# Kernel tuning notes

Hardware: AMD Instinct MI355X
Metric: run time of the kernel (lower is better)

## Reference

```python
import jax, jax.numpy as jnp
import numpy as np

EMB = 1024   # embedding_size = input_size // 2
HID = 1024   # hidden_size
B = 16384


def _glorot(key, shape):
    fan_in = shape[0]
    bound = 1.0 / np.sqrt(fan_in)
    return jax.random.uniform(key, shape, jnp.float32, -bound, bound)


def setup_inputs() -> dict:
    key = jax.random.key(0)
    ks = jax.random.split(key, 14)
    return {
        "inputs": jax.random.normal(ks[0], (B, 2 * EMB), jnp.float32),
        "state": jax.random.normal(ks[1], (B, HID), jnp.float32),
        # weights stored [in, out] (transpose of torch Linear layout)
        "Wr": _glorot(ks[2], (EMB + HID, HID)), "br": jnp.zeros((HID,), jnp.float32),
        "Wu": _glorot(ks[3], (EMB + HID, HID)), "bu": jnp.zeros((HID,), jnp.float32),
        "Wc": _glorot(ks[4], (EMB + HID, HID)), "bc": jnp.zeros((HID,), jnp.float32),
        "W1": _glorot(ks[5], (EMB, HID)), "b1": jnp.zeros((HID,), jnp.float32),
        "W2": _glorot(ks[6], (EMB, HID)), "b2": jnp.zeros((HID,), jnp.float32),
        "Wg": _glorot(ks[7], (2 * HID, HID)), "bg": jnp.zeros((HID,), jnp.float32),
    }


def reference(inputs, state, Wr, br, Wu, bu, Wc, bc, W1, b1, W2, b2, Wg, bg):
    # split input into semantic half and neighbor half
    x = inputs[:, :EMB]          # [B, EMB]
    neighbors = inputs[:, EMB:]  # [B, EMB]

    gate_inputs = jnp.concatenate([x, state], axis=1)            # [B, EMB+HID]
    r = jax.nn.sigmoid(gate_inputs @ Wr + br)                    # reset gate
    u = jax.nn.sigmoid(gate_inputs @ Wu + bu)                    # update gate
    c = jnp.tanh(jnp.concatenate([x, r * state], axis=1) @ Wc + bc)

    semantic_emb = jax.nn.relu(x @ W1 + b1)
    neighbor_emb = jax.nn.relu(neighbors @ W2 + b2)
    new_gate = jax.nn.sigmoid(
        jnp.concatenate([semantic_emb, neighbor_emb], axis=1) @ Wg + bg)

    new_h = u * state + (1.0 - u) * c * new_gate
    return new_h
```

## Files before the change

### kernel.cpp

```cpp
#include <hip/hip_runtime.h>
#include <hip/hip_bf16.h>
#include <math.h>

#define Bsz 16384
#define HIDc 1024

typedef __attribute__((ext_vector_type(8))) short short8_t;
typedef __attribute__((ext_vector_type(4))) float f32x4;
typedef __attribute__((ext_vector_type(4))) short s16x4;

typedef __attribute__((address_space(1))) const unsigned char* gp1_t;
typedef __attribute__((address_space(3))) unsigned char* lp3_t;

__device__ __forceinline__ float sigf(float x) { return 1.0f / (1.0f + __expf(-x)); }
__device__ __forceinline__ float tanh_fast(float x) {
  x = fminf(fmaxf(x, -10.f), 10.f);
  float t = __expf(2.f * x);
  return (t - 1.f) / (t + 1.f);
}

__device__ __forceinline__ int xcd_map(int bid, int nwg) {
  const int q = nwg >> 3, r = nwg & 7;
  const int xcd = bid & 7, idx = bid >> 3;
  return (xcd < r ? xcd * (q + 1) : r * (q + 1) + (xcd - r) * q) + idx;
}

#define DSR(dst, addr, IMM) \
  asm volatile("ds_read_b128 %0, %1 offset:" IMM : "=v"(dst) : "v"(addr))

#define STAGE_ADV(BUFB) do {                                                                     \
    __hip_bfloat16* db_ = lds + (BUFB);                                                          \
    __builtin_amdgcn_global_load_lds((gp1_t)pa0, (lp3_t)(db_ + tid * 8), 16, 0, 0);              \
    __builtin_amdgcn_global_load_lds((gp1_t)pa1, (lp3_t)(db_ + (512 + tid) * 8), 16, 0, 0);      \
    __builtin_amdgcn_global_load_lds((gp1_t)pa2, (lp3_t)(db_ + (1024 + tid) * 8), 16, 0, 0);     \
    __builtin_amdgcn_global_load_lds((gp1_t)pa3, (lp3_t)(db_ + (1536 + tid) * 8), 16, 0, 0);     \
    __builtin_amdgcn_global_load_lds((gp1_t)pb0, (lp3_t)(db_ + 16384 + tid * 8), 16, 0, 0);      \
    __builtin_amdgcn_global_load_lds((gp1_t)pb1, (lp3_t)(db_ + 16384 + (512 + tid) * 8), 16, 0, 0); \
    __builtin_amdgcn_global_load_lds((gp1_t)pb2, (lp3_t)(db_ + 16384 + (1024 + tid) * 8), 16, 0, 0); \
    __builtin_amdgcn_global_load_lds((gp1_t)pb3, (lp3_t)(db_ + 16384 + (1536 + tid) * 8), 16, 0, 0); \
    pa0 += 64; pa1 += 64; pa2 += 64; pa3 += 64;                                                  \
    pb0 += 64; pb1 += 64; pb2 += 64; pb3 += 64;                                                  \
  } while (0)

template <int EPI>
__global__ __launch_bounds__(512, 2)
void gemm256(const __hip_bfloat16* __restrict__ A, long lda,
             const __hip_bfloat16* __restrict__ Wt, long ldw, int nbx,
             const float* __restrict__ bias0, const float* __restrict__ bias1,
             const __hip_bfloat16* __restrict__ stbf,
             const __hip_bfloat16* __restrict__ auxbf,
             const __hip_bfloat16* __restrict__ CB,
             const __hip_bfloat16* __restrict__ U,
             __hip_bfloat16* __restrict__ out0,
             __hip_bfloat16* __restrict__ out1,
             float* __restrict__ outf) {
  constexpr int KC = (EPI == 0 || EPI == 4) ? 2048 : 1024;
  constexpr int NS = KC / 64;
  __shared__ __hip_bfloat16 lds[2 * 32768];

  const int tid = threadIdx.x;
  const int wave = tid >> 6, lane = tid & 63;
  const int wr = wave >> 2, wc = wave & 3;
  const int lm = lane & 15, hi = lane >> 4, l7 = lane & 7;

  const int wg = xcd_map(blockIdx.x, gridDim.x);
  const long mBase = (long)(wg / nbx) * 256;
  const long nBase = (long)(wg % nbx) * 256;
  const __hip_bfloat16* Ablk = A + mBase * lda;
  const __hip_bfloat16* Wblk = Wt + nBase * ldw;

  const __hip_bfloat16 *pa0, *pa1, *pa2, *pa3, *pb0, *pb1, *pb2, *pb3;
  {
    const int s0 = tid, s1 = 512 + tid, s2 = 1024 + tid, s3 = 1536 + tid;
    const int r0 = s0 >> 3, r1 = s1 >> 3, r2 = s2 >> 3, r3 = s3 >> 3;
    const int c0 = ((s0 & 7) ^ (r0 & 7)) << 3, c1 = ((s1 & 7) ^ (r1 & 7)) << 3;
    const int c2 = ((s2 & 7) ^ (r2 & 7)) << 3, c3 = ((s3 & 7) ^ (r3 & 7)) << 3;
    pa0 = Ablk + (long)r0 * lda + c0;  pa1 = Ablk + (long)r1 * lda + c1;
    pa2 = Ablk + (long)r2 * lda + c2;  pa3 = Ablk + (long)r3 * lda + c3;
    pb0 = Wblk + (long)r0 * ldw + c0;  pb1 = Wblk + (long)r1 * ldw + c1;
    pb2 = Wblk + (long)r2 * ldw + c2;  pb3 = Wblk + (long)r3 * ldw + c3;
  }

  const unsigned ldsbase = (unsigned)(size_t)(void*)lds;
  const unsigned laneA = (unsigned)((wr * 128 + lm) * 128 + ((hi ^ l7) << 4));
  const unsigned laneB = (unsigned)(32768 + (wc * 64 + lm) * 128 + ((hi ^ l7) << 4));

  f32x4 acc[8][4];
#pragma unroll
  for (int m = 0; m < 8; ++m)
#pragma unroll
    for (int n = 0; n < 4; ++n) acc[m][n] = (f32x4){0.f, 0.f, 0.f, 0.f};

  STAGE_ADV(0);
  STAGE_ADV(32768);

#pragma unroll 1
  for (int s = 0; s < NS; ++s) {
    if (s == NS - 1) asm volatile("s_waitcnt vmcnt(0)" ::: "memory");
    else             asm volatile("s_waitcnt vmcnt(8)" ::: "memory");
    __builtin_amdgcn_s_barrier();

    const unsigned base = ldsbase + (unsigned)((s & 1) * 65536);
    const unsigned a0 = base + laneA, b0 = base + laneB;
    const unsigned a1 = a0 ^ 64u, b1 = b0 ^ 64u;
    short8_t a8[8], b8[4];

    DSR(a8[0], a0, "0");    DSR(a8[1], a0, "2048");  DSR(a8[2], a0, "4096");
    DSR(a8[3], a0, "6144"); DSR(a8[4], a0, "8192");  DSR(a8[5], a0, "10240");
    DSR(a8[6], a0, "12288");DSR(a8[7], a0, "14336");
    DSR(b8[0], b0, "0");    DSR(b8[1], b0, "2048");  DSR(b8[2], b0, "4096");
    DSR(b8[3], b0, "6144");
    asm volatile("s_waitcnt lgkmcnt(0)" ::: "memory");
    __builtin_amdgcn_sched_barrier(0);
    __builtin_amdgcn_s_setprio(1);
#pragma unroll
    for (int mf = 0; mf < 8; ++mf)
#pragma unroll
      for (int nf = 0; nf < 4; ++nf)
        acc[mf][nf] = __builtin_amdgcn_mfma_f32_16x16x32_bf16(a8[mf], b8[nf],
                                                              acc[mf][nf], 0, 0, 0);
    __builtin_amdgcn_s_setprio(0);

    DSR(a8[0], a1, "0");    DSR(a8[1], a1, "2048");  DSR(a8[2], a1, "4096");
    DSR(a8[3], a1, "6144"); DSR(a8[4], a1, "8192");  DSR(a8[5], a1, "10240");
    DSR(a8[6], a1, "12288");DSR(a8[7], a1, "14336");
    DSR(b8[0], b1, "0");    DSR(b8[1], b1, "2048");  DSR(b8[2], b1, "4096");
    DSR(b8[3], b1, "6144");
    asm volatile("s_waitcnt lgkmcnt(0)" ::: "memory");
    __builtin_amdgcn_sched_barrier(0);
    __builtin_amdgcn_s_barrier();
    __builtin_amdgcn_sched_barrier(0);
    if (s + 2 < NS) STAGE_ADV((s & 1) * 32768);
    __builtin_amdgcn_s_setprio(1);
#pragma unroll
    for (int mf = 0; mf < 8; ++mf)
#pragma unroll
      for (int nf = 0; nf < 4; ++nf)
        acc[mf][nf] = __builtin_amdgcn_mfma_f32_16x16x32_bf16(a8[mf], b8[nf],
                                                              acc[mf][nf], 0, 0, 0);
    __builtin_amdgcn_s_setprio(0);
  }

#pragma unroll
  for (int mf = 0; mf < 8; ++mf)
#pragma unroll
    for (int nf = 0; nf < 4; ++nf)
#pragma unroll
      for (int j = 0; j < 4; ++j) {
        const long row = mBase + wr * 128 + mf * 16 + hi * 4 + j;
        const int col = (int)nBase + wc * 64 + nf * 16 + lm;
        const float v = acc[mf][nf][j];
        if (EPI == 0) {
          if (col < HIDc) {
            float rr = sigf(v + bias0[col]);
            float st = __bfloat162float(stbf[row * 2048 + 1024 + col]);
            out0[row * HIDc + col] = __float2bfloat16(rr * st);
          } else {
            int c = col - HIDc;
            out1[row * HIDc + c] = __float2bfloat16(sigf(v + bias1[c]));
          }
        } else if (EPI == 1) {
          if (col < HIDc) {
            out0[row * 2048 + col] = __float2bfloat16(fmaxf(v + bias0[col], 0.f));
          } else {
            int c = col - HIDc;
            out1[row * HIDc + c] = __float2bfloat16(v + bias1[c]);
          }
        } else if (EPI == 2) {
          out0[row * 2048 + HIDc + col] = __float2bfloat16(fmaxf(v + bias0[col], 0.f));
        } else if (EPI == 3) {
          const long idx = row * HIDc + col;
          out0[idx] = __float2bfloat16(tanh_fast(v + __bfloat162float(auxbf[idx])));
        } else {
          const long idx = row * HIDc + col;
          float g = sigf(v + bias0[col]);
          float u = __bfloat162float(U[idx]);
          float cb = __bfloat162float(CB[idx]);
          float st = __bfloat162float(stbf[row * 2048 + 1024 + col]);
          outf[idx] = u * st + (1.f - u) * cb * g;
        }
      }
}

__global__ __launch_bounds__(256)
void prep_k(const float4* __restrict__ in4, const float4* __restrict__ st4,
            __hip_bfloat16* __restrict__ A1, __hip_bfloat16* __restrict__ NB,
            const float* __restrict__ Wr, const float* __restrict__ Wu,
            const float* __restrict__ W1, const float* __restrict__ Wc,
            const float* __restrict__ W2, const float* __restrict__ Wg,
            __hip_bfloat16* __restrict__ Wru_t, __hip_bfloat16* __restrict__ W1cx_t,
            __hip_bfloat16* __restrict__ Wcb_t, __hip_bfloat16* __restrict__ W2_t,
            __hip_bfloat16* __restrict__ Wg_t) {
  const int bid = blockIdx.x;
  if (bid < 10240) {
    const float* s_; __hip_bfloat16* d_; long ldo; int j, ktiles;
    if (bid < 2048)      { j = bid;        s_ = Wr; d_ = Wru_t;               ldo = 2048; ktiles = 64; }
    else if (bid < 4096) { j = bid - 2048; s_ = Wu; d_ = Wru_t + 1024L * 2048; ldo = 2048; ktiles = 64; }
    else if (bid < 5120) { j = bid - 4096; s_ = W1; d_ = W1cx_t;              ldo = 1024; ktiles = 32; }
    else if (bid < 6144) { j = bid - 5120; s_ = Wc; d_ = W1cx_t + 1024L * 1024; ldo = 1024; ktiles = 32; }
    else if (bid < 7168) { j = bid - 6144; s_ = Wc + 1024L * 1024; d_ = Wcb_t; ldo = 1024; ktiles = 32; }
    else if (bid < 8192) { j = bid - 7168; s_ = W2; d_ = W2_t;                ldo = 1024; ktiles = 32; }
    else                 { j = bid - 8192; s_ = Wg; d_ = Wg_t;                ldo = 2048; ktiles = 64; }
    const int k0 = (j % ktiles) * 32, n0 = (j / ktiles) * 32;
    __shared__ float t[32][33];
    const int tx = threadIdx.x & 31, ty = threadIdx.x >> 5;
#pragma unroll
    for (int dy = 0; dy < 32; dy += 8)
      t[ty + dy][tx] = s_[(long)(k0 + ty + dy) * 1024 + n0 + tx];
    __syncthreads();
#pragma unroll
    for (int dy = 0; dy < 32; dy += 8)
      d_[(long)(n0 + ty + dy) * ldo + k0 + tx] = __float2bfloat16(t[tx][ty + dy]);
  } else {
    const long NI4 = (long)Bsz * 2048 / 4;
    const long NS4 = (long)Bsz * 1024 / 4;
    for (long i = (long)(bid - 10240) * 256 + threadIdx.x; i < NI4 + NS4;
         i += 2048L * 256) {
      float4 v;
      __hip_bfloat16* dst;
      if (i < NI4) {
        v = in4[i];
        long e = i << 2;
        long row = e >> 11;
        int col = (int)(e & 2047);
        dst = (col < 1024) ? (A1 + row * 2048 + col) : (NB + row * 1024 + (col - 1024));
      } else {
        long jj = i - NI4;
        v = st4[jj];
        long e = jj << 2;
        long row = e >> 10;
        int col = (int)(e & 1023);
        dst = A1 + row * 2048 + 1024 + col;
      }
      union { __hip_bfloat16 h[4]; s16x4 s; } u;
      u.h[0] = __float2bfloat16(v.x);
      u.h[1] = __float2bfloat16(v.y);
      u.h[2] = __float2bfloat16(v.z);
      u.h[3] = __float2bfloat16(v.w);
      *reinterpret_cast<s16x4*>(dst) = u.s;
    }
  }
}

extern "C" void kernel_launch(void* const* d_in, const int* in_sizes, int n_in,
                              void* d_out, int out_size, void* d_ws, size_t ws_size,
                              hipStream_t stream) {
  const float* inputs = (const float*)d_in[0];
  const float* state = (const float*)d_in[1];
  const float* Wr = (const float*)d_in[2];
  const float* br = (const float*)d_in[3];
  const float* Wu = (const float*)d_in[4];
  const float* bu = (const float*)d_in[5];
  const float* Wc = (const float*)d_in[6];
  const float* bc = (const float*)d_in[7];
  const float* W1 = (const float*)d_in[8];
  const float* b1 = (const float*)d_in[9];
  const float* W2 = (const float*)d_in[10];
  const float* b2 = (const float*)d_in[11];
  const float* Wg = (const float*)d_in[12];
  const float* bg = (const float*)d_in[13];
  float* out = (float*)d_out;

  char* ws = (char*)d_ws;
  __hip_bfloat16* A1    = (__hip_bfloat16*)(ws);
  __hip_bfloat16* NB    = (__hip_bfloat16*)(ws + 67108864L);
  __hip_bfloat16* RS    = (__hip_bfloat16*)(ws + 100663296L);
  __hip_bfloat16* Ub    = (__hip_bfloat16*)(ws + 134217728L);
  __hip_bfloat16* SN    = (__hip_bfloat16*)(ws + 167772160L);
  __hip_bfloat16* CXb   = (__hip_bfloat16*)(ws + 234881024L);
  __hip_bfloat16* Wru_t = (__hip_bfloat16*)(ws + 268435456L);
  __hip_bfloat16* W1cx_t= (__hip_bfloat16*)(ws + 276824064L);
  __hip_bfloat16* Wcb_t = (__hip_bfloat16*)(ws + 281018368L);
  __hip_bfloat16* W2_t  = (__hip_bfloat16*)(ws + 283115520L);
  __hip_bfloat16* Wg_t  = (__hip_bfloat16*)(ws + 285212672L);
  __hip_bfloat16* CB    = NB;

  prep_k<<<12288, 256, 0, stream>>>((const float4*)inputs, (const float4*)state,
                                    A1, NB, Wr, Wu, W1, Wc, W2, Wg,
                                    Wru_t, W1cx_t, Wcb_t, W2_t, Wg_t);

  gemm256<0><<<512, 512, 0, stream>>>(A1, 2048, Wru_t, 2048, 8,
                                      br, bu, A1, nullptr, nullptr, nullptr,
                                      RS, Ub, nullptr);
  gemm256<1><<<512, 512, 0, stream>>>(A1, 2048, W1cx_t, 1024, 8,
                                      b1, bc, nullptr, nullptr, nullptr, nullptr,
                                      SN, CXb, nullptr);
  gemm256<2><<<256, 512, 0, stream>>>(NB, 1024, W2_t, 1024, 4,
                                      b2, nullptr, nullptr, nullptr, nullptr, nullptr,
                                      SN, nullptr, nullptr);
  gemm256<3><<<256, 512, 0, stream>>>(RS, 1024, Wcb_t, 1024, 4,
                                      nullptr, nullptr, nullptr, CXb, nullptr, nullptr,
                                      CB, nullptr, nullptr);
  gemm256<4><<<256, 512, 0, stream>>>(SN, 2048, Wg_t, 2048, 4,
                                      bg, nullptr, A1, nullptr, CB, Ub,
                                      nullptr, nullptr, out);
}
```

Before: 522.4 us.

## Split GEMM main loop into four quadrant MFMA phases with interleaved LDS reads

Restructures the K-loop of the 256x256 GEMM so each stage runs as four quadrant MFMA blocks (over M and N halves), each covering both K sub-steps. LDS fragment reads for the next quadrant sit between barriers, and the global prefetch is issued before the last quadrant. The aim is to overlap LDS reads with MFMA work across waves and to move the vmcnt wait to the end of the iteration. The cost is many more workgroup barriers per iteration and more live fragment registers.

```diff
diff --git a/kernel.cpp b/kernel.cpp
--- a/kernel.cpp
+++ b/kernel.cpp
@@ -40,6 +40,21 @@
     __builtin_amdgcn_global_load_lds((gp1_t)pb3, (lp3_t)(db_ + 16384 + (1536 + tid) * 8), 16, 0, 0); \
     pa0 += 64; pa1 += 64; pa2 += 64; pa3 += 64;                                                  \
     pb0 += 64; pb1 += 64; pb2 += 64; pb3 += 64;                                                  \
+  } while (0)
+
+#define MFMA_Q(QM, QN) do {                                                      \
+    asm volatile("s_waitcnt lgkmcnt(0)" ::: "memory");                           \
+    __builtin_amdgcn_sched_barrier(0);                                           \
+    __builtin_amdgcn_s_setprio(1);                                               \
+    _Pragma("unroll") for (int ks = 0; ks < 2; ++ks)                             \
+      _Pragma("unroll") for (int mf = 0; mf < 4; ++mf)                           \
+        _Pragma("unroll") for (int nf = 0; nf < 2; ++nf)                         \
+          acc[(QM) * 4 + mf][(QN) * 2 + nf] =                                    \
+              __builtin_amdgcn_mfma_f32_16x16x32_bf16(                           \
+                  a8[mf][ks], b8[QN][nf][ks],                                    \
+                  acc[(QM) * 4 + mf][(QN) * 2 + nf], 0, 0, 0);                   \
+    __builtin_amdgcn_s_setprio(0);                                               \
+    __builtin_amdgcn_sched_barrier(0);                                           \
   } while (0)
 
 template <int EPI>
@@ -91,54 +106,49 @@
 #pragma unroll
     for (int n = 0; n < 4; ++n) acc[m][n] = (f32x4){0.f, 0.f, 0.f, 0.f};
 
+  short8_t a8[4][2], b8[2][2][2];
+
   STAGE_ADV(0);
   STAGE_ADV(32768);
+  asm volatile("s_waitcnt vmcnt(8)" ::: "memory");
+  __builtin_amdgcn_s_barrier();
 
 #pragma unroll 1
   for (int s = 0; s < NS; ++s) {
-    if (s == NS - 1) asm volatile("s_waitcnt vmcnt(0)" ::: "memory");
-    else             asm volatile("s_waitcnt vmcnt(8)" ::: "memory");
-    __builtin_amdgcn_s_barrier();
-
     const unsigned base = ldsbase + (unsigned)((s & 1) * 65536);
     const unsigned a0 = base + laneA, b0 = base + laneB;
     const unsigned a1 = a0 ^ 64u, b1 = b0 ^ 64u;
-    short8_t a8[8], b8[4];
-
-    DSR(a8[0], a0, "0");    DSR(a8[1], a0, "2048");  DSR(a8[2], a0, "4096");
-    DSR(a8[3], a0, "6144"); DSR(a8[4], a0, "8192");  DSR(a8[5], a0, "10240");
-    DSR(a8[6], a0, "12288");DSR(a8[7], a0, "14336");
-    DSR(b8[0], b0, "0");    DSR(b8[1], b0, "2048");  DSR(b8[2], b0, "4096");
-    DSR(b8[3], b0, "6144");
-    asm volatile("s_waitcnt lgkmcnt(0)" ::: "memory");
-    __builtin_amdgcn_sched_barrier(0);
-    __builtin_amdgcn_s_setprio(1);
-#pragma unroll
-    for (int mf = 0; mf < 8; ++mf)
-#pragma unroll
-      for (int nf = 0; nf < 4; ++nf)
-        acc[mf][nf] = __builtin_amdgcn_mfma_f32_16x16x32_bf16(a8[mf], b8[nf],
-                                                              acc[mf][nf], 0, 0, 0);
-    __builtin_amdgcn_s_setprio(0);
-
-    DSR(a8[0], a1, "0");    DSR(a8[1], a1, "2048");  DSR(a8[2], a1, "4096");
-    DSR(a8[3], a1, "6144"); DSR(a8[4], a1, "8192");  DSR(a8[5], a1, "10240");
-    DSR(a8[6], a1, "12288");DSR(a8[7], a1, "14336");
-    DSR(b8[0], b1, "0");    DSR(b8[1], b1, "2048");  DSR(b8[2], b1, "4096");
-    DSR(b8[3], b1, "6144");
-    asm volatile("s_waitcnt lgkmcnt(0)" ::: "memory");
-    __builtin_amdgcn_sched_barrier(0);
-    __builtin_amdgcn_s_barrier();
-    __builtin_amdgcn_sched_barrier(0);
+
+    DSR(a8[0][0], a0, "0"); DSR(a8[1][0], a0, "2048");
+    DSR(a8[2][0], a0, "4096"); DSR(a8[3][0], a0, "6144");
+    DSR(a8[0][1], a1, "0"); DSR(a8[1][1], a1, "2048");
+    DSR(a8[2][1], a1, "4096"); DSR(a8[3][1], a1, "6144");
+    DSR(b8[0][0][0], b0, "0"); DSR(b8[0][1][0], b0, "2048");
+    DSR(b8[0][0][1], b1, "0"); DSR(b8[0][1][1], b1, "2048");
+    __builtin_amdgcn_s_barrier();
+    MFMA_Q(0, 0);
+    __builtin_amdgcn_s_barrier();
+
+    DSR(b8[1][0][0], b0, "4096"); DSR(b8[1][1][0], b0, "6144");
+    DSR(b8[1][0][1], b1, "4096"); DSR(b8[1][1][1], b1, "6144");
+    __builtin_amdgcn_s_barrier();
+    MFMA_Q(0, 1);
+    __builtin_amdgcn_s_barrier();
+
+    DSR(a8[0][0], a0, "8192"); DSR(a8[1][0], a0, "10240");
+    DSR(a8[2][0], a0, "12288"); DSR(a8[3][0], a0, "14336");
+    DSR(a8[0][1], a1, "8192"); DSR(a8[1][1], a1, "10240");
+    DSR(a8[2][1], a1, "12288"); DSR(a8[3][1], a1, "14336");
+    __builtin_amdgcn_s_barrier();
+    MFMA_Q(1, 0);
+    __builtin_amdgcn_s_barrier();
+
     if (s + 2 < NS) STAGE_ADV((s & 1) * 32768);
-    __builtin_amdgcn_s_setprio(1);
-#pragma unroll
-    for (int mf = 0; mf < 8; ++mf)
-#pragma unroll
-      for (int nf = 0; nf < 4; ++nf)
-        acc[mf][nf] = __builtin_amdgcn_mfma_f32_16x16x32_bf16(a8[mf], b8[nf],
-                                                              acc[mf][nf], 0, 0, 0);
-    __builtin_amdgcn_s_setprio(0);
+    __builtin_amdgcn_s_barrier();
+    MFMA_Q(1, 1);
+    if (s + 2 < NS) asm volatile("s_waitcnt vmcnt(8)" ::: "memory");
+    else            asm volatile("s_waitcnt vmcnt(0)" ::: "memory");
+    __builtin_amdgcn_s_barrier();
   }
 
 #pragma unroll
```

Result: slower. 568.6 us (+8.8%).

## Merge independent GEMMs into one launch and split K-loop into finer pipelined phases

Applied to the files above, without the earlier changes.

The three independent first-stage GEMMs (reset/update, semantic/candidate-x, neighbor) are merged into a single grouped kernel launch, so the tail of one no longer idles the GPU before the next starts and there are fewer launches. The shared GEMM core is restructured into four sub-phases per K step, each reading a quarter of the fragments and issuing part of the next stage's global-to-LDS loads. This interleaves memory traffic with MFMA work at finer granularity and cuts live fragment registers, at the cost of more barriers per iteration and runtime branching on the epilogue type.

```diff
diff --git a/kernel.cpp b/kernel.cpp
--- a/kernel.cpp
+++ b/kernel.cpp
@@ -28,119 +28,133 @@
 #define DSR(dst, addr, IMM) \
   asm volatile("ds_read_b128 %0, %1 offset:" IMM : "=v"(dst) : "v"(addr))
 
-#define STAGE_ADV(BUFB) do {                                                                     \
-    __hip_bfloat16* db_ = lds + (BUFB);                                                          \
-    __builtin_amdgcn_global_load_lds((gp1_t)pa0, (lp3_t)(db_ + tid * 8), 16, 0, 0);              \
-    __builtin_amdgcn_global_load_lds((gp1_t)pa1, (lp3_t)(db_ + (512 + tid) * 8), 16, 0, 0);      \
-    __builtin_amdgcn_global_load_lds((gp1_t)pa2, (lp3_t)(db_ + (1024 + tid) * 8), 16, 0, 0);     \
-    __builtin_amdgcn_global_load_lds((gp1_t)pa3, (lp3_t)(db_ + (1536 + tid) * 8), 16, 0, 0);     \
-    __builtin_amdgcn_global_load_lds((gp1_t)pb0, (lp3_t)(db_ + 16384 + tid * 8), 16, 0, 0);      \
-    __builtin_amdgcn_global_load_lds((gp1_t)pb1, (lp3_t)(db_ + 16384 + (512 + tid) * 8), 16, 0, 0); \
-    __builtin_amdgcn_global_load_lds((gp1_t)pb2, (lp3_t)(db_ + 16384 + (1024 + tid) * 8), 16, 0, 0); \
-    __builtin_amdgcn_global_load_lds((gp1_t)pb3, (lp3_t)(db_ + 16384 + (1536 + tid) * 8), 16, 0, 0); \
-    pa0 += 64; pa1 += 64; pa2 += 64; pa3 += 64;                                                  \
-    pb0 += 64; pb1 += 64; pb2 += 64; pb3 += 64;                                                  \
-  } while (0)
-
-template <int EPI>
-__global__ __launch_bounds__(512, 2)
-void gemm256(const __hip_bfloat16* __restrict__ A, long lda,
-             const __hip_bfloat16* __restrict__ Wt, long ldw, int nbx,
-             const float* __restrict__ bias0, const float* __restrict__ bias1,
-             const __hip_bfloat16* __restrict__ stbf,
-             const __hip_bfloat16* __restrict__ auxbf,
-             const __hip_bfloat16* __restrict__ CB,
-             const __hip_bfloat16* __restrict__ U,
-             __hip_bfloat16* __restrict__ out0,
-             __hip_bfloat16* __restrict__ out1,
-             float* __restrict__ outf) {
-  constexpr int KC = (EPI == 0 || EPI == 4) ? 2048 : 1024;
-  constexpr int NS = KC / 64;
-  __shared__ __hip_bfloat16 lds[2 * 32768];
-
-  const int tid = threadIdx.x;
-  const int wave = tid >> 6, lane = tid & 63;
+#define GLL(P, T, DST) \
+  __builtin_amdgcn_global_load_lds((gp1_t)((P) + (long)(T) * 64), (lp3_t)(DST), 16, 0, 0)
+
+#define MFMA16(QM, QN)                                                           \
+  _Pragma("unroll") for (int ks = 0; ks < 2; ++ks)                               \
+    _Pragma("unroll") for (int mf = 0; mf < 4; ++mf)                             \
+      _Pragma("unroll") for (int nf = 0; nf < 2; ++nf)                           \
+        acc[(QM) * 4 + mf][(QN) * 2 + nf] =                                      \
+            __builtin_amdgcn_mfma_f32_16x16x32_bf16(                             \
+                a8[mf][ks], b8[QN][nf][ks], acc[(QM) * 4 + mf][(QN) * 2 + nf], 0, 0, 0)
+
+__device__ __forceinline__ void g256_core(const __hip_bfloat16* __restrict__ Ablk, long lda,
+                                          const __hip_bfloat16* __restrict__ Wblk, long ldw,
+                                          int NS, __hip_bfloat16* lds, f32x4 (&acc)[8][4],
+                                          int tid, int wave, int lane) {
   const int wr = wave >> 2, wc = wave & 3;
   const int lm = lane & 15, hi = lane >> 4, l7 = lane & 7;
-
-  const int wg = xcd_map(blockIdx.x, gridDim.x);
-  const long mBase = (long)(wg / nbx) * 256;
-  const long nBase = (long)(wg % nbx) * 256;
-  const __hip_bfloat16* Ablk = A + mBase * lda;
-  const __hip_bfloat16* Wblk = Wt + nBase * ldw;
-
-  const __hip_bfloat16 *pa0, *pa1, *pa2, *pa3, *pb0, *pb1, *pb2, *pb3;
-  {
-    const int s0 = tid, s1 = 512 + tid, s2 = 1024 + tid, s3 = 1536 + tid;
-    const int r0 = s0 >> 3, r1 = s1 >> 3, r2 = s2 >> 3, r3 = s3 >> 3;
-    const int c0 = ((s0 & 7) ^ (r0 & 7)) << 3, c1 = ((s1 & 7) ^ (r1 & 7)) << 3;
-    const int c2 = ((s2 & 7) ^ (r2 & 7)) << 3, c3 = ((s3 & 7) ^ (r3 & 7)) << 3;
-    pa0 = Ablk + (long)r0 * lda + c0;  pa1 = Ablk + (long)r1 * lda + c1;
-    pa2 = Ablk + (long)r2 * lda + c2;  pa3 = Ablk + (long)r3 * lda + c3;
-    pb0 = Wblk + (long)r0 * ldw + c0;  pb1 = Wblk + (long)r1 * ldw + c1;
-    pb2 = Wblk + (long)r2 * ldw + c2;  pb3 = Wblk + (long)r3 * ldw + c3;
-  }
+  const int s0 = tid, s1 = 512 + tid, s2 = 1024 + tid, s3 = 1536 + tid;
+  const int r0 = s0 >> 3, r1 = s1 >> 3, r2 = s2 >> 3, r3 = s3 >> 3;
+  const int c0 = ((s0 & 7) ^ (r0 & 7)) << 3, c1 = ((s1 & 7) ^ (r1 & 7)) << 3;
+  const int c2 = ((s2 & 7) ^ (r2 & 7)) << 3, c3 = ((s3 & 7) ^ (r3 & 7)) << 3;
+  const __hip_bfloat16* pa0 = Ablk + (long)r0 * lda + c0;
+  const __hip_bfloat16* pa1 = Ablk + (long)r1 * lda + c1;
+  const __hip_bfloat16* pa2 = Ablk + (long)r2 * lda + c2;
+  const __hip_bfloat16* pa3 = Ablk + (long)r3 * lda + c3;
+  const __hip_bfloat16* pb0 = Wblk + (long)r0 * ldw + c0;
+  const __hip_bfloat16* pb1 = Wblk + (long)r1 * ldw + c1;
+  const __hip_bfloat16* pb2 = Wblk + (long)r2 * ldw + c2;
+  const __hip_bfloat16* pb3 = Wblk + (long)r3 * ldw + c3;
 
   const unsigned ldsbase = (unsigned)(size_t)(void*)lds;
   const unsigned laneA = (unsigned)((wr * 128 + lm) * 128 + ((hi ^ l7) << 4));
   const unsigned laneB = (unsigned)(32768 + (wc * 64 + lm) * 128 + ((hi ^ l7) << 4));
 
-  f32x4 acc[8][4];
-#pragma unroll
-  for (int m = 0; m < 8; ++m)
-#pragma unroll
-    for (int n = 0; n < 4; ++n) acc[m][n] = (f32x4){0.f, 0.f, 0.f, 0.f};
-
-  STAGE_ADV(0);
-  STAGE_ADV(32768);
-
+  GLL(pa0, 0, lds + tid * 8);                 GLL(pa1, 0, lds + (512 + tid) * 8);
+  GLL(pa2, 0, lds + (1024 + tid) * 8);        GLL(pa3, 0, lds + (1536 + tid) * 8);
+  GLL(pb0, 0, lds + 16384 + tid * 8);         GLL(pb1, 0, lds + 16384 + (512 + tid) * 8);
+  GLL(pb2, 0, lds + 16384 + (1024 + tid) * 8);GLL(pb3, 0, lds + 16384 + (1536 + tid) * 8);
+  GLL(pb0, 1, lds + 49152 + tid * 8);         GLL(pb1, 1, lds + 49152 + (512 + tid) * 8);
+  GLL(pb2, 1, lds + 49152 + (1024 + tid) * 8);GLL(pb3, 1, lds + 49152 + (1536 + tid) * 8);
+  asm volatile("s_waitcnt vmcnt(4)" ::: "memory");
+  __builtin_amdgcn_s_barrier();
+
+  short8_t a8[4][2], b8[2][2][2];
 #pragma unroll 1
   for (int s = 0; s < NS; ++s) {
-    if (s == NS - 1) asm volatile("s_waitcnt vmcnt(0)" ::: "memory");
-    else             asm volatile("s_waitcnt vmcnt(8)" ::: "memory");
-    __builtin_amdgcn_s_barrier();
-
     const unsigned base = ldsbase + (unsigned)((s & 1) * 65536);
     const unsigned a0 = base + laneA, b0 = base + laneB;
     const unsigned a1 = a0 ^ 64u, b1 = b0 ^ 64u;
-    short8_t a8[8], b8[4];
-
-    DSR(a8[0], a0, "0");    DSR(a8[1], a0, "2048");  DSR(a8[2], a0, "4096");
-    DSR(a8[3], a0, "6144"); DSR(a8[4], a0, "8192");  DSR(a8[5], a0, "10240");
-    DSR(a8[6], a0, "12288");DSR(a8[7], a0, "14336");
-    DSR(b8[0], b0, "0");    DSR(b8[1], b0, "2048");  DSR(b8[2], b0, "4096");
-    DSR(b8[3], b0, "6144");
+    __hip_bfloat16* nA = lds + ((s + 1) & 1) * 32768;
+    __hip_bfloat16* cB = lds + (s & 1) * 32768 + 16384;
+
+    DSR(a8[0][0], a0, "0");    DSR(a8[1][0], a0, "2048");
+    DSR(a8[2][0], a0, "4096"); DSR(a8[3][0], a0, "6144");
+    DSR(a8[0][1], a1, "0");    DSR(a8[1][1], a1, "2048");
+    DSR(a8[2][1], a1, "4096"); DSR(a8[3][1], a1, "6144");
+    DSR(b8[0][0][0], b0, "0"); DSR(b8[0][1][0], b0, "2048");
+    DSR(b8[0][0][1], b1, "0"); DSR(b8[0][1][1], b1, "2048");
+    if (s + 1 < NS) { GLL(pa0, s + 1, nA + tid * 8); GLL(pa1, s + 1, nA + (512 + tid) * 8); }
+    __builtin_amdgcn_s_barrier();
     asm volatile("s_waitcnt lgkmcnt(0)" ::: "memory");
     __builtin_amdgcn_sched_barrier(0);
-    __builtin_amdgcn_s_setprio(1);
-#pragma unroll
-    for (int mf = 0; mf < 8; ++mf)
-#pragma unroll
-      for (int nf = 0; nf < 4; ++nf)
-        acc[mf][nf] = __builtin_amdgcn_mfma_f32_16x16x32_bf16(a8[mf], b8[nf],
-                                                              acc[mf][nf], 0, 0, 0);
-    __builtin_amdgcn_s_setprio(0);
-
-    DSR(a8[0], a1, "0");    DSR(a8[1], a1, "2048");  DSR(a8[2], a1, "4096");
-    DSR(a8[3], a1, "6144"); DSR(a8[4], a1, "8192");  DSR(a8[5], a1, "10240");
-    DSR(a8[6], a1, "12288");DSR(a8[7], a1, "14336");
-    DSR(b8[0], b1, "0");    DSR(b8[1], b1, "2048");  DSR(b8[2], b1, "4096");
-    DSR(b8[3], b1, "6144");
+    __builtin_amdgcn_s_setprio(1); MFMA16(0, 0); __builtin_amdgcn_s_setprio(0);
+    __builtin_amdgcn_s_barrier();
+
+    DSR(b8[1][0][0], b0, "4096"); DSR(b8[1][1][0], b0, "6144");
+    DSR(b8[1][0][1], b1, "4096"); DSR(b8[1][1][1], b1, "6144");
+    if (s + 1 < NS) { GLL(pa2, s + 1, nA + (1024 + tid) * 8); GLL(pa3, s + 1, nA + (1536 + tid) * 8); }
+    __builtin_amdgcn_s_barrier();
     asm volatile("s_waitcnt lgkmcnt(0)" ::: "memory");
     __builtin_amdgcn_sched_barrier(0);
-    __builtin_amdgcn_s_barrier();
+    __builtin_amdgcn_s_setprio(1); MFMA16(0, 1); __builtin_amdgcn_s_setprio(0);
+    __builtin_amdgcn_s_barrier();
+
+    DSR(a8[0][0], a0, "8192");  DSR(a8[1][0], a0, "10240");
+    DSR(a8[2][0], a0, "12288"); DSR(a8[3][0], a0, "14336");
+    DSR(a8[0][1], a1, "8192");  DSR(a8[1][1], a1, "10240");
+    DSR(a8[2][1], a1, "12288"); DSR(a8[3][1], a1, "14336");
+    if (s + 2 < NS) { GLL(pb0, s + 2, cB + tid * 8); GLL(pb1, s + 2, cB + (512 + tid) * 8); }
+    __builtin_amdgcn_s_barrier();
+    asm volatile("s_waitcnt lgkmcnt(0)" ::: "memory");
     __builtin_amdgcn_sched_barrier(0);
-    if (s + 2 < NS) STAGE_ADV((s & 1) * 32768);
-    __builtin_amdgcn_s_setprio(1);
-#pragma unroll
-    for (int mf = 0; mf < 8; ++mf)
-#pragma unroll
-      for (int nf = 0; nf < 4; ++nf)
-        acc[mf][nf] = __builtin_amdgcn_mfma_f32_16x16x32_bf16(a8[mf], b8[nf],
-                                                              acc[mf][nf], 0, 0, 0);
-    __builtin_amdgcn_s_setprio(0);
+    __builtin_amdgcn_s_setprio(1); MFMA16(1, 0); __builtin_amdgcn_s_setprio(0);
+    __builtin_amdgcn_s_barrier();
+
+    if (s + 2 < NS) { GLL(pb2, s + 2, cB + (1024 + tid) * 8); GLL(pb3, s + 2, cB + (1536 + tid) * 8); }
+    __builtin_amdgcn_s_barrier();
+    __builtin_amdgcn_s_setprio(1); MFMA16(1, 1); __builtin_amdgcn_s_setprio(0);
+    if (s + 2 < NS)      asm volatile("s_waitcnt vmcnt(4)" ::: "memory");
+    else if (s + 1 < NS) asm volatile("s_waitcnt vmcnt(0)" ::: "memory");
+    __builtin_amdgcn_s_barrier();
   }
-
+}
+
+__global__ __launch_bounds__(512, 2)
+void mega256(const __hip_bfloat16* __restrict__ A1,
+             const __hip_bfloat16* __restrict__ NB,
+             const __hip_bfloat16* __restrict__ Wru,
+             const __hip_bfloat16* __restrict__ W1cx,
+             const __hip_bfloat16* __restrict__ W2t,
+             const float* __restrict__ br, const float* __restrict__ bu,
+             const float* __restrict__ b1, const float* __restrict__ bc,
+             const float* __restrict__ b2,
+             __hip_bfloat16* __restrict__ RS, __hip_bfloat16* __restrict__ Ub,
+             __hip_bfloat16* __restrict__ SN, __hip_bfloat16* __restrict__ CXb) {
+  __shared__ __hip_bfloat16 lds[2 * 32768];
+  const int bid = blockIdx.x;
+  const __hip_bfloat16 *A, *Wt;
+  long lda, ldw;
+  int NS, nbx, epi, local, seg;
+  if (bid < 512)        { local = bid;        seg = 512; epi = 0; A = A1; lda = 2048; Wt = Wru;  ldw = 2048; NS = 32; nbx = 8; }
+  else if (bid < 1024)  { local = bid - 512;  seg = 512; epi = 1; A = A1; lda = 2048; Wt = W1cx; ldw = 1024; NS = 16; nbx = 8; }
+  else                  { local = bid - 1024; seg = 256; epi = 2; A = NB; lda = 1024; Wt = W2t;  ldw = 1024; NS = 16; nbx = 4; }
+  const int wg = xcd_map(local, seg);
+  const long mBase = (long)(wg / nbx) * 256;
+  const long nBase = (long)(wg % nbx) * 256;
+
+  f32x4 acc[8][4];
+#pragma unroll
+  for (int m = 0; m < 8; ++m)
+#pragma unroll
+    for (int n = 0; n < 4; ++n) acc[m][n] = (f32x4){0.f, 0.f, 0.f, 0.f};
+
+  const int tid = threadIdx.x, wave = tid >> 6, lane = tid & 63;
+  g256_core(A + mBase * lda, lda, Wt + nBase * ldw, ldw, NS, lds, acc, tid, wave, lane);
+
+  const int wr = wave >> 2, wc = wave & 3, lm = lane & 15, hi = lane >> 4;
 #pragma unroll
   for (int mf = 0; mf < 8; ++mf)
 #pragma unroll
@@ -150,35 +164,98 @@
         const long row = mBase + wr * 128 + mf * 16 + hi * 4 + j;
         const int col = (int)nBase + wc * 64 + nf * 16 + lm;
         const float v = acc[mf][nf][j];
-        if (EPI == 0) {
+        if (epi == 0) {
           if (col < HIDc) {
-            float rr = sigf(v + bias0[col]);
-            float st = __bfloat162float(stbf[row * 2048 + 1024 + col]);
-            out0[row * HIDc + col] = __float2bfloat16(rr * st);
+            float rr = sigf(v + br[col]);
+            float st = __bfloat162float(A1[row * 2048 + 1024 + col]);
+            RS[row * HIDc + col] = __float2bfloat16(rr * st);
           } else {
             int c = col - HIDc;
-            out1[row * HIDc + c] = __float2bfloat16(sigf(v + bias1[c]));
+            Ub[row * HIDc + c] = __float2bfloat16(sigf(v + bu[c]));
           }
-        } else if (EPI == 1) {
+        } else if (epi == 1) {
           if (col < HIDc) {
-            out0[row * 2048 + col] = __float2bfloat16(fmaxf(v + bias0[col], 0.f));
+            SN[row * 2048 + col] = __float2bfloat16(fmaxf(v + b1[col], 0.f));
           } else {
             int c = col - HIDc;
-            out1[row * HIDc + c] = __float2bfloat16(v + bias1[c]);
+            CXb[row * HIDc + c] = __float2bfloat16(v + bc[c]);
           }
-        } else if (EPI == 2) {
-          out0[row * 2048 + HIDc + col] = __float2bfloat16(fmaxf(v + bias0[col], 0.f));
-        } else if (EPI == 3) {
-          const long idx = row * HIDc + col;
-          out0[idx] = __float2bfloat16(tanh_fast(v + __bfloat162float(auxbf[idx])));
         } else {
-          const long idx = row * HIDc + col;
-          float g = sigf(v + bias0[col]);
-          float u = __bfloat162float(U[idx]);
-          float cb = __bfloat162float(CB[idx]);
-          float st = __bfloat162float(stbf[row * 2048 + 1024 + col]);
-          outf[idx] = u * st + (1.f - u) * cb * g;
+          SN[row * 2048 + HIDc + col] = __float2bfloat16(fmaxf(v + b2[col], 0.f));
         }
+      }
+}
+
+__global__ __launch_bounds__(512, 2)
+void final_c256(const __hip_bfloat16* __restrict__ RS,
+                const __hip_bfloat16* __restrict__ Wcb,
+                const __hip_bfloat16* __restrict__ CXb,
+                __hip_bfloat16* __restrict__ CB) {
+  __shared__ __hip_bfloat16 lds[2 * 32768];
+  const int wg = xcd_map(blockIdx.x, gridDim.x);
+  const long mBase = (long)(wg / 4) * 256;
+  const long nBase = (long)(wg % 4) * 256;
+
+  f32x4 acc[8][4];
+#pragma unroll
+  for (int m = 0; m < 8; ++m)
+#pragma unroll
+    for (int n = 0; n < 4; ++n) acc[m][n] = (f32x4){0.f, 0.f, 0.f, 0.f};
+
+  const int tid = threadIdx.x, wave = tid >> 6, lane = tid & 63;
+  g256_core(RS + mBase * HIDc, HIDc, Wcb + nBase * HIDc, HIDc, 16, lds, acc, tid, wave, lane);
+
+  const int wr = wave >> 2, wc = wave & 3, lm = lane & 15, hi = lane >> 4;
+#pragma unroll
+  for (int mf = 0; mf < 8; ++mf)
+#pragma unroll
+    for (int nf = 0; nf < 4; ++nf)
+#pragma unroll
+      for (int j = 0; j < 4; ++j) {
+        const long row = mBase + wr * 128 + mf * 16 + hi * 4 + j;
+        const int col = (int)nBase + wc * 64 + nf * 16 + lm;
+        const long idx = row * HIDc + col;
+        CB[idx] = __float2bfloat16(tanh_fast(acc[mf][nf][j] + __bfloat162float(CXb[idx])));
+      }
+}
+
+__global__ __launch_bounds__(512, 2)
+void final_g256(const __hip_bfloat16* __restrict__ SN,
+                const __hip_bfloat16* __restrict__ Wgt,
+                const __hip_bfloat16* __restrict__ CB,
+                const __hip_bfloat16* __restrict__ U,
+                const __hip_bfloat16* __restrict__ stbf,
+                const float* __restrict__ bg,
+                float* __restrict__ out) {
+  __shared__ __hip_bfloat16 lds[2 * 32768];
+  const int wg = xcd_map(blockIdx.x, gridDim.x);
+  const long mBase = (long)(wg / 4) * 256;
+  const long nBase = (long)(wg % 4) * 256;
+
+  f32x4 acc[8][4];
+#pragma unroll
+  for (int m = 0; m < 8; ++m)
+#pragma unroll
+    for (int n = 0; n < 4; ++n) acc[m][n] = (f32x4){0.f, 0.f, 0.f, 0.f};
+
+  const int tid = threadIdx.x, wave = tid >> 6, lane = tid & 63;
+  g256_core(SN + mBase * 2048, 2048, Wgt + nBase * 2048, 2048, 32, lds, acc, tid, wave, lane);
+
+  const int wr = wave >> 2, wc = wave & 3, lm = lane & 15, hi = lane >> 4;
+#pragma unroll
+  for (int mf = 0; mf < 8; ++mf)
+#pragma unroll
+    for (int nf = 0; nf < 4; ++nf)
+#pragma unroll
+      for (int j = 0; j < 4; ++j) {
+        const long row = mBase + wr * 128 + mf * 16 + hi * 4 + j;
+        const int col = (int)nBase + wc * 64 + nf * 16 + lm;
+        const long idx = row * HIDc + col;
+        float g = sigf(acc[mf][nf][j] + bg[col]);
+        float u = __bfloat162float(U[idx]);
+        float cb = __bfloat162float(CB[idx]);
+        float st = __bfloat162float(stbf[row * 2048 + 1024 + col]);
+        out[idx] = u * st + (1.f - u) * cb * g;
       }
 }
 
@@ -279,19 +356,11 @@
                                     A1, NB, Wr, Wu, W1, Wc, W2, Wg,
                                     Wru_t, W1cx_t, Wcb_t, W2_t, Wg_t);
 
-  gemm256<0><<<512, 512, 0, stream>>>(A1, 2048, Wru_t, 2048, 8,
-                                      br, bu, A1, nullptr, nullptr, nullptr,
-                                      RS, Ub, nullptr);
-  gemm256<1><<<512, 512, 0, stream>>>(A1, 2048, W1cx_t, 1024, 8,
-                                      b1, bc, nullptr, nullptr, nullptr, nullptr,
-                                      SN, CXb, nullptr);
-  gemm256<2><<<256, 512, 0, stream>>>(NB, 1024, W2_t, 1024, 4,
-                                      b2, nullptr, nullptr, nullptr, nullptr, nullptr,
-                                      SN, nullptr, nullptr);
-  gemm256<3><<<256, 512, 0, stream>>>(RS, 1024, Wcb_t, 1024, 4,
-                                      nullptr, nullptr, nullptr, CXb, nullptr, nullptr,
-                                      CB, nullptr, nullptr);
-  gemm256<4><<<256, 512, 0, stream>>>(SN, 2048, Wg_t, 2048, 4,
-                                      bg, nullptr, A1, nullptr, CB, Ub,
-                                      nullptr, nullptr, out);
-}
+  mega256<<<1280, 512, 0, stream>>>(A1, NB, Wru_t, W1cx_t, W2_t,
+                                    br, bu, b1, bc, b2,
+                                    RS, Ub, SN, CXb);
+
+  final_c256<<<256, 512, 0, stream>>>(RS, Wcb_t, CXb, CB);
+
+  final_g256<<<256, 512, 0, stream>>>(SN, Wg_t, CB, Ub, A1, bg, out);
+}
```

Measured after the change: 521.9 us. About the same (-0.1%).
